# Kernel tuning notes

Hardware: AMD Instinct MI355X
Metric: run time of the kernel (lower is better)

Reference implementation:

```python
import jax, jax.numpy as jnp
import numpy as np

B, S = 32, 256


def _lsa(cost):
    """Rectangular linear sum assignment (Jonker-Volgenant shortest augmenting path),
    equivalent to scipy.optimize.linear_sum_assignment. cost: [R, C] numpy."""
    cost = np.asarray(cost, dtype=np.float64)
    transposed = cost.shape[0] > cost.shape[1]
    if transposed:
        cost = cost.T
    nr, nc = cost.shape  # nr <= nc
    u = np.zeros(nr)
    v = np.zeros(nc)
    path = np.full(nc, -1, dtype=np.int64)
    col4row = np.full(nr, -1, dtype=np.int64)
    row4col = np.full(nc, -1, dtype=np.int64)
    for cur_row in range(nr):
        min_val = 0.0
        i = cur_row
        remaining = np.arange(nc)
        sp = np.full(nc, np.inf)
        SR = np.zeros(nr, dtype=bool)
        SC = np.zeros(nc, dtype=bool)
        sink = -1
        while sink == -1:
            SR[i] = True
            r = min_val + cost[i, remaining] - u[i] - v[remaining]
            better = r < sp[remaining]
            idx_b = remaining[better]
            sp[idx_b] = r[better]
            path[idx_b] = i
            k = int(np.argmin(sp[remaining]))
            j = int(remaining[k])
            min_val = float(sp[j])
            if row4col[j] == -1:
                sink = j
            else:
                i = int(row4col[j])
                SC[j] = True
                remaining = np.delete(remaining, k)
        u[cur_row] += min_val
        others = SR.copy()
        others[cur_row] = False
        rr = np.where(others)[0]
        u[rr] += min_val - sp[col4row[rr]]
        cc = np.where(SC)[0]
        v[cc] += sp[cc] - min_val
        j = sink
        while True:
            i = int(path[j])
            row4col[j] = i
            col4row[i], j = j, int(col4row[i])
            if i == cur_row:
                break
    if transposed:
        rows = col4row
        cols = np.arange(nr)
        order = np.argsort(rows)
        return rows[order], cols[order]
    return np.arange(nr), col4row


def _match(cost_np, valid_np):
    """Per-sample Hungarian matching restricted to valid GT columns.
    Returns padded (pred_idx, gt_idx) [B, maxG] and ngt [B]."""
    Bn = cost_np.shape[0]
    ngt = valid_np.sum(axis=1).astype(np.int64)
    maxG = max(int(ngt.max()), 1)
    pi = np.zeros((Bn, maxG), dtype=np.int64)
    gi = np.zeros((Bn, maxG), dtype=np.int64)
    for b in range(Bn):
        cols = np.where(valid_np[b])[0]
        if len(cols) == 0:
            continue
        r, c = _lsa(cost_np[b][:, cols])
        pi[b, : len(r)] = r
        gi[b, : len(c)] = cols[c]
    return pi, gi, ngt


def _bce_clipped(p, t):
    # matches torch BCELoss: log terms clamped at -100
    return -(t * jnp.clip(jnp.log(p), -100.0) + (1.0 - t) * jnp.clip(jnp.log(1.0 - p), -100.0))


def _loss(pred_strokes, pred_validity, targets, pi, gi, ngt):
    gt_strokes = targets[..., :10]
    gt_val = targets[..., 10:11]
    Bn, maxG = pi.shape
    ngt_f = jnp.asarray(ngt, dtype=pred_strokes.dtype)
    mask = (jnp.arange(maxG)[None, :] < jnp.asarray(ngt)[:, None]).astype(pred_strokes.dtype)  # [B, maxG]
    bidx = np.arange(Bn)[:, None]
    mp = pred_strokes[bidx, pi]  # [B, maxG, 10]
    mg = gt_strokes[bidx, gi]    # [B, maxG, 10]
    # per-sample L1 means over matched pairs (coord: first 8 dims, width: last 2)
    coord = (jnp.abs(mp[..., :8] - mg[..., :8]).sum(-1) * mask).sum(-1) / jnp.maximum(ngt_f * 8.0, 1.0)
    width = (jnp.abs(mp[..., 8:10] - mg[..., 8:10]).sum(-1) * mask).sum(-1) / jnp.maximum(ngt_f * 2.0, 1.0)
    bce = _bce_clipped(pred_validity, gt_val).mean(axis=(1, 2))  # global validity BCE per sample
    # if num_gt == 0 the original only adds the validity BCE
    loss_b = jnp.where(ngt_f > 0, 5.0 * coord + 1.0 * width + 1.0 * bce, bce)
    return loss_b.mean()


def setup_inputs() -> dict:
    key = jax.random.key(0)
    k1, k2, k3, k4 = jax.random.split(key, 4)
    pred_strokes = jax.random.normal(k1, (B, S, 10), dtype=jnp.float32)
    pred_validity = jax.random.uniform(k2, (B, S, 1), dtype=jnp.float32, minval=1e-4, maxval=1.0 - 1e-4)
    gt_strokes = jax.random.normal(k3, (B, S, 10), dtype=jnp.float32)
    gt_valid = (jax.random.uniform(k4, (B, S, 1)) < 0.3).astype(jnp.float32)
    targets = jnp.concatenate([gt_strokes, gt_valid], axis=-1)
    return {"pred_strokes": pred_strokes, "pred_validity": pred_validity, "targets": targets}


def reference(pred_strokes, pred_validity, targets):
    gt_strokes = targets[..., :10]
    gt_val = targets[..., 10:11]
    # vectorized pairwise cost: 5 * L1(coord) + 1 * L1(width), [B, S, S]
    coord_c = jnp.abs(pred_strokes[:, :, None, :8] - gt_strokes[:, None, :, :8]).sum(-1)
    width_c = jnp.abs(pred_strokes[:, :, None, 8:10] - gt_strokes[:, None, :, 8:10]).sum(-1)
    cost = 5.0 * coord_c + width_c
    pi, gi, ngt = _match(np.asarray(cost), np.asarray(gt_val[..., 0]) > 0.5)
    return _loss(pred_strokes, pred_validity, targets, pi, gi, ngt)
```

## Files before the change

### kernel.cpp

```cpp
#include <hip/hip_runtime.h>
#include <math.h>

#define BN 32
#define SN 256
#define CAP 96
#define NT  256

#define KINF 0xFF800000u
#define KMAX 0xFFFFFFFFu
#define CLNONE 0x7FFFFFFF

__device__ __forceinline__ unsigned f2k(float f) {
    unsigned b = __float_as_uint(f);
    return (b & 0x80000000u) ? ~b : (b | 0x80000000u);
}
__device__ __forceinline__ float k2f(unsigned k) {
    unsigned b = (k & 0x80000000u) ? (k ^ 0x80000000u) : ~k;
    return __uint_as_float(b);
}
__device__ __forceinline__ int sel4(int a0, int a1, int a2, int a3, int s) {
    int x01 = (s & 1) ? a1 : a0;
    int x23 = (s & 1) ? a3 : a2;
    return (s & 2) ? x23 : x01;
}
#define DPP_MIN(x, ctrl) do {                                                    \
    unsigned _t = (unsigned)__builtin_amdgcn_update_dpp((int)(x), (int)(x),      \
                                                        (ctrl), 0xF, 0xF, false);\
    if (_t < (x)) (x) = _t;                                                      \
} while (0)
#define DPP_MIN2(m1, m2, ctrl) do {                                              \
    unsigned _o1 = (unsigned)__builtin_amdgcn_update_dpp(-1, (int)(m1),          \
                                                         (ctrl), 0xF, 0xF, false);\
    unsigned _o2 = (unsigned)__builtin_amdgcn_update_dpp(-1, (int)(m2),          \
                                                         (ctrl), 0xF, 0xF, false);\
    unsigned _hi = (m1) > _o1 ? (m1) : _o1;                                      \
    (m1) = (m1) < _o1 ? (m1) : _o1;                                              \
    unsigned _s  = (m2) < _o2 ? (m2) : _o2;                                      \
    (m2) = _s < _hi ? _s : _hi;                                                  \
} while (0)
#define DPP_CHAIN_MIN2(a,b) do { DPP_MIN2(a,b,0x111); DPP_MIN2(a,b,0x112); DPP_MIN2(a,b,0x114); \
                                 DPP_MIN2(a,b,0x118); DPP_MIN2(a,b,0x142); DPP_MIN2(a,b,0x143); } while (0)

__device__ __forceinline__ unsigned waveMinU(unsigned x) {
    DPP_MIN(x, 0x111);
    DPP_MIN(x, 0x112);
    DPP_MIN(x, 0x114);
    DPP_MIN(x, 0x118);
    DPP_MIN(x, 0x142);
    DPP_MIN(x, 0x143);
    return (unsigned)__builtin_amdgcn_readlane((int)x, 63);
}

__device__ __forceinline__ void pickLowest(unsigned long long n0, unsigned long long n1,
                                           unsigned long long n2, unsigned long long n3,
                                           int& lm, int& slot) {
    int l0 = n0 ? __builtin_ctzll(n0) : 64;
    int l1 = n1 ? __builtin_ctzll(n1) : 64;
    int l2 = n2 ? __builtin_ctzll(n2) : 64;
    int l3 = n3 ? __builtin_ctzll(n3) : 64;
    int a  = l0 < l1 ? l0 : l1;
    int c  = l2 < l3 ? l2 : l3;
    lm   = a < c ? a : c;
    slot = (l0 == lm) ? 0 : (l1 == lm) ? 1 : (l2 == lm) ? 2 : 3;
}

__device__ __forceinline__ void waveArgmin(unsigned q0, unsigned q1, unsigned q2,
                                           unsigned q3, unsigned& vk, int& col) {
    unsigned a = q0 < q1 ? q0 : q1;
    unsigned b = q2 < q3 ? q2 : q3;
    unsigned m = a < b ? a : b;
    vk = waveMinU(m);
    unsigned long long n0 = __ballot(q0 == vk);
    unsigned long long n1 = __ballot(q1 == vk);
    unsigned long long n2 = __ballot(q2 == vk);
    unsigned long long n3 = __ballot(q3 == vk);
    int lm, slot;
    pickLowest(n0, n1, n2, n3, lm, slot);
    col = lm * 4 + slot;
}

__device__ __forceinline__ float costf(const float* pb, const float* gc) {
    float c = 0.f;
    #pragma unroll
    for (int d = 0; d < 8; ++d) c += fabsf(pb[d] - gc[d]);
    float w = fabsf(pb[8] - gc[8]) + fabsf(pb[9] - gc[9]);
    return 5.0f * c + w;
}

__global__ __launch_bounds__(NT) void detr_kernel(
    const float* __restrict__ pred_strokes,
    const float* __restrict__ pred_validity,
    const float* __restrict__ targets,
    float* __restrict__ out)
{
    extern __shared__ __align__(16) float sC[];
    __shared__ __align__(16) float sPred[SN * 10];
    __shared__ __align__(16) float sRowC[SN * 10];
    __shared__ float sU[SN];
    __shared__ float sVal[SN];
    __shared__ int   sJ[SN];
    __shared__ int   sClaim[SN];
    __shared__ int   sFree[SN];
    __shared__ int   sCr4[SN];
    __shared__ float sRed[12];
    __shared__ int   sNgt;

    const int b = blockIdx.x, tid = threadIdx.x, lane = tid & 63, wid = tid >> 6;

    {
        const float4* gp = (const float4*)(pred_strokes + (size_t)b * SN * 10);
        float4* sp4 = (float4*)sPred;
        for (int t = tid; t < SN * 10 / 4; t += NT) sp4[t] = gp[t];
        const float4* gt = (const float4*)(targets + (size_t)b * SN * 11);
        float4* st4 = (float4*)sC;
        for (int t = tid; t < SN * 11 / 4; t += NT) st4[t] = gt[t];
        sClaim[tid] = CLNONE;
        sJ[tid]     = 0;
    }
    __syncthreads();

    if (wid == 0) {
        const float* tmpT = sC;
        int ng = 0;
        #pragma unroll
        for (int s = 0; s < 4; ++s) {
            int   pos = s * 64 + lane;
            float tv  = tmpT[pos * 11 + 10];
            sVal[pos] = tv;
            bool  val = tv > 0.5f;
            unsigned long long m = __ballot(val);
            if (val) {
                int r = ng + (int)__popcll(m & ((1ull << lane) - 1ull));
                #pragma unroll
                for (int d = 0; d < 10; ++d) sRowC[r * 10 + d] = tmpT[pos * 11 + d];
            }
            ng += (int)__popcll(m);
        }
        if (lane == 0) sNgt = ng;
    }
    __syncthreads();
    const int ngt = sNgt;

    __align__(16) float prf[40];
    #pragma unroll
    for (int t = 0; t < 10; ++t) ((float4*)prf)[t] = ((const float4*)sPred)[lane * 10 + t];

    float bces;
    {
        float pv  = pred_validity[(size_t)b * SN + tid];
        float tv  = sVal[tid];
        float lp  = logf(pv);       if (lp  < -100.f) lp  = -100.f;
        float l1p = logf(1.f - pv); if (l1p < -100.f) l1p = -100.f;
        bces = -(tv * lp + (1.f - tv) * l1p);
    }

    for (int r = wid; r < ngt; r += 4) {
        const float* gp = &sRowC[r * 10];
        float gc[10];
        #pragma unroll
        for (int d = 0; d < 10; ++d) gc[d] = gp[d];
        float4 cc;
        cc.x = costf(prf +  0, gc);
        cc.y = costf(prf + 10, gc);
        cc.z = costf(prf + 20, gc);
        cc.w = costf(prf + 30, gc);
        if (r < CAP) ((float4*)sC)[r * 64 + lane] = cc;

        unsigned q0 = f2k(cc.x), q1 = f2k(cc.y), q2 = f2k(cc.z), q3 = f2k(cc.w);
        unsigned u1k; int mj;
        waveArgmin(q0, q1, q2, q3, u1k, mj);
        if (lane == 0) {
            sU[r] = k2f(u1k);
            sJ[r] = mj;
            atomicMin(&sClaim[mj], r);
        }
    }
    __syncthreads();

    if (wid == 0) {
        float v0 = 0.f, v1 = 0.f, v2 = 0.f, v3 = 0.f;
        float sc0 = 0.f, sc1 = 0.f, sc2 = 0.f, sc3 = 0.f;
        int   p0 = -1, p1 = -1, p2 = -1, p3 = -1;

        int4 cl = ((const int4*)sClaim)[lane];
        int rv0 = (cl.x != CLNONE) ? cl.x : -1;
        int rv1 = (cl.y != CLNONE) ? cl.y : -1;
        int rv2 = (cl.z != CLNONE) ? cl.z : -1;
        int rv3 = (cl.w != CLNONE) ? cl.w : -1;
        int4 j4 = ((const int4*)sJ)[lane];
        int cr0 = (lane * 4 + 0 < ngt && sClaim[j4.x] == lane * 4 + 0) ? j4.x : -1;
        int cr1 = (lane * 4 + 1 < ngt && sClaim[j4.y] == lane * 4 + 1) ? j4.y : -1;
        int cr2 = (lane * 4 + 2 < ngt && sClaim[j4.z] == lane * 4 + 2) ? j4.z : -1;
        int cr3 = (lane * 4 + 3 < ngt && sClaim[j4.w] == lane * 4 + 3) ? j4.w : -1;

        int nfree = 0;
        #pragma unroll
        for (int s = 0; s < 4; ++s) {
            int  pos = s * 64 + lane;
            bool fr = (pos < ngt) && (sClaim[sJ[pos]] != pos);
            unsigned long long m = __ballot(fr);
            if (fr) sFree[nfree + (int)__popcll(m & ((1ull << lane) - 1ull))] = pos;
            nfree += (int)__popcll(m);
        }

        #define ASSIGN_COL(J, R) { unsigned _m = (lane == ((J) >> 2)) ? (1u << ((J) & 3)) : 0u; \
            rv0 = (_m & 1) ? (R) : rv0; rv1 = (_m & 2) ? (R) : rv1;                             \
            rv2 = (_m & 4) ? (R) : rv2; rv3 = (_m & 8) ? (R) : rv3; }
        #define ASSIGN_ROW(R, J) { unsigned _m = (lane == ((R) >> 2)) ? (1u << ((R) & 3)) : 0u; \
            cr0 = (_m & 1) ? (J) : cr0; cr1 = (_m & 2) ? (J) : cr1;                             \
            cr2 = (_m & 4) ? (J) : cr2; cr3 = (_m & 8) ? (J) : cr3; }
        #define READ_RV(LM, SL) __builtin_amdgcn_readlane(sel4(rv0,rv1,rv2,rv3,(SL)), (LM))
        #define LOADROW(I, CW)                                                   \
            if ((I) < CAP) (CW) = ((const float4*)sC)[(I) * 64 + lane];          \
            else {                                                               \
                float gc[10];                                                    \
                _Pragma("unroll")                                                \
                for (int d = 0; d < 10; ++d) gc[d] = sRowC[(I) * 10 + d];        \
                (CW).x = costf(prf +  0, gc); (CW).y = costf(prf + 10, gc);      \
                (CW).z = costf(prf + 20, gc); (CW).w = costf(prf + 30, gc);      \
            }

        int cnt = nfree;
        for (int pass = 0; pass < 2 && cnt > 0; ++pass) {
            int newc = 0;
            int rN = sFree[0];
            float4 cwN;
            LOADROW(rN, cwN)
            for (int idx = 0; idx < cnt; ++idx) {
                const int r = rN;
                const float4 cw = cwN;
                if (idx + 1 < cnt) {
                    rN = sFree[idx + 1];
                    LOADROW(rN, cwN)
                }
                unsigned q0 = f2k(cw.x - v0), q1 = f2k(cw.y - v1);
                unsigned q2 = f2k(cw.z - v2), q3 = f2k(cw.w - v3);
                unsigned a1 = q0 < q1 ? q0 : q1, a2 = q0 < q1 ? q1 : q0;
                unsigned b1 = q2 < q3 ? q2 : q3, b2 = q2 < q3 ? q3 : q2;
                unsigned m1 = a1 < b1 ? a1 : b1;
                unsigned hi = a1 < b1 ? b1 : a1;
                unsigned l2 = a2 < b2 ? a2 : b2;
                unsigned m2 = l2 < hi ? l2 : hi;
                DPP_CHAIN_MIN2(m1, m2);
                unsigned u1k = (unsigned)__builtin_amdgcn_readlane((int)m1, 63);
                unsigned u2k = (unsigned)__builtin_amdgcn_readlane((int)m2, 63);

                unsigned long long n0 = __ballot(q0 == u1k);
                unsigned long long n1 = __ballot(q1 == u1k);
                unsigned long long n2 = __ballot(q2 == u1k);
                unsigned long long n3 = __ballot(q3 == u1k);
                int lm, slot;
                pickLowest(n0, n1, n2, n3, lm, slot);
                int j1 = lm * 4 + slot;
                int i1 = READ_RV(lm, slot);

                if (u1k != u2k) {
                    float du = k2f(u1k) - k2f(u2k);
                    unsigned _m = (lane == (j1 >> 2)) ? (1u << (j1 & 3)) : 0u;
                    v0 = (_m & 1) ? v0 + du : v0;
                    v1 = (_m & 2) ? v1 + du : v1;
                    v2 = (_m & 4) ? v2 + du : v2;
                    v3 = (_m & 8) ? v3 + du : v3;
                    if (lane == 0) sU[r] = k2f(u2k);
                } else {
                    if (i1 >= 0) {
                        switch (slot) {
                            case 0:  n0 &= ~(1ull << lm); break;
                            case 1:  n1 &= ~(1ull << lm); break;
                            case 2:  n2 &= ~(1ull << lm); break;
                            default: n3 &= ~(1ull << lm); break;
                        }
                        pickLowest(n0, n1, n2, n3, lm, slot);
                        j1 = lm * 4 + slot;
                        i1 = READ_RV(lm, slot);
                    }
                    if (lane == 0) sU[r] = k2f(u1k);
                }

                ASSIGN_COL(j1, r)
                ASSIGN_ROW(r, j1)
                if (i1 >= 0) {
                    if (lane == 0) sFree[newc] = i1;
                    newc++;
                }
            }
            cnt = newc;
        }

        for (int fi = 0; fi < cnt; ++fi) {
            const int cur = sFree[fi];
            unsigned k0 = KINF, k1 = KINF, k2 = KINF, k3 = KINF;
            int   scm  = 0;
            float minv = 0.f;
            int   i    = cur;
            int   sink;

            float4 cw;
            LOADROW(i, cw)
            float ui = sU[i];

            for (;;) {
                #define RELAX(S, CS, KS, PS, VS)                                 \
                {                                                                \
                    float rr = ((minv + CS) - ui) - VS;                          \
                    unsigned kr = f2k(rr);                                       \
                    bool upd = (kr < KS) && !((scm >> S) & 1);                   \
                    if (upd) { KS = kr; PS = i; }                                \
                }
                RELAX(0, cw.x, k0, p0, v0)
                RELAX(1, cw.y, k1, p1, v1)
                RELAX(2, cw.z, k2, p2, v2)
                RELAX(3, cw.w, k3, p3, v3)
                #undef RELAX

                unsigned vk; int bj;
                waveArgmin(k0, k1, k2, k3, vk, bj);
                int lm = bj >> 2, slot = bj & 3;
                int rn = READ_RV(lm, slot);
                minv = k2f(vk);
                if (rn < 0) { sink = bj; break; }
                i = rn;

                float4 cw2;
                LOADROW(i, cw2)
                float ui2 = sU[i];

                unsigned _m = (lane == lm) ? (1u << slot) : 0u;
                scm |= (int)_m;
                k0 = (_m & 1) ? KMAX : k0;  sc0 = (_m & 1) ? minv : sc0;
                k1 = (_m & 2) ? KMAX : k1;  sc1 = (_m & 2) ? minv : sc1;
                k2 = (_m & 4) ? KMAX : k2;  sc2 = (_m & 4) ? minv : sc2;
                k3 = (_m & 8) ? KMAX : k3;  sc3 = (_m & 8) ? minv : sc3;

                cw = cw2; ui = ui2;
            }

            if (lane == 0) sU[cur] += minv;
            if (scm & 1) { sU[rv0] += minv - sc0; v0 += sc0 - minv; }
            if (scm & 2) { sU[rv1] += minv - sc1; v1 += sc1 - minv; }
            if (scm & 4) { sU[rv2] += minv - sc2; v2 += sc2 - minv; }
            if (scm & 8) { sU[rv3] += minv - sc3; v3 += sc3 - minv; }

            int j = sink;
            for (;;) {
                int sj = j & 3, lj = j >> 2;
                int i2 = __builtin_amdgcn_readlane(sel4(p0, p1, p2, p3, sj), lj);
                ASSIGN_COL(j, i2)
                int si = i2 & 3, li = i2 >> 2;
                int tmp = __builtin_amdgcn_readlane(sel4(cr0, cr1, cr2, cr3, si), li);
                ASSIGN_ROW(i2, j)
                j = tmp;
                if (i2 == cur) break;
            }
        }

        ((int4*)sCr4)[lane] = make_int4(cr0, cr1, cr2, cr3);
    }
    __syncthreads();

    float coordv = 0.f, widthv = 0.f;
    if (tid < ngt) {
        int p = sCr4[tid];
        const float* pp = &sPred[p * 10];
        const float* gg = &sRowC[tid * 10];
        float c = 0.f;
        #pragma unroll
        for (int d = 0; d < 8; ++d) c += fabsf(pp[d] - gg[d]);
        coordv = c;
        widthv = fabsf(pp[8] - gg[8]) + fabsf(pp[9] - gg[9]);
    }
    #pragma unroll
    for (int m = 1; m <= 32; m <<= 1) {
        coordv += __shfl_xor(coordv, m, 64);
        widthv += __shfl_xor(widthv, m, 64);
        bces   += __shfl_xor(bces,   m, 64);
    }
    if (lane == 0) {
        sRed[wid * 3 + 0] = coordv;
        sRed[wid * 3 + 1] = widthv;
        sRed[wid * 3 + 2] = bces;
    }
    __syncthreads();
    if (tid == 0) {
        float C = 0.f, W = 0.f, Bc = 0.f;
        #pragma unroll
        for (int w = 0; w < 4; ++w) {
            C += sRed[w * 3 + 0]; W += sRed[w * 3 + 1]; Bc += sRed[w * 3 + 2];
        }
        float bcem = Bc / (float)SN;
        float lb = (ngt > 0)
                 ? (5.f * C / (8.f * (float)ngt) + W / (2.f * (float)ngt) + bcem)
                 : bcem;
        atomicAdd(out, lb * (1.0f / (float)BN));
    }
}

extern "C" void kernel_launch(void* const* d_in, const int* in_sizes, int n_in,
                              void* d_out, int out_size, void* d_ws, size_t ws_size,
                              hipStream_t stream) {
    const float* pred_strokes  = (const float*)d_in[0];
    const float* pred_validity = (const float*)d_in[1];
    const float* targets       = (const float*)d_in[2];
    float* out = (float*)d_out;

    const int dynBytes = CAP * SN * 4;
    (void)hipFuncSetAttribute((const void*)detr_kernel,
                              hipFuncAttributeMaxDynamicSharedMemorySize, dynBytes);
    detr_kernel<<<BN, NT, dynBytes, stream>>>(pred_strokes, pred_validity, targets, out);
}
```

Baseline: 115.4 us.

## Use native float min reductions and restructure JV relax to shorten critical path

Replaces the order-preserving uint key encoding (f2k/k2f) with direct float fminf/fmaxf in the DPP wave reductions and argmin ballots. It also restructures the shortest-augmenting-path inner loop: per-row reduced costs (b0..b3) and their lane minimum are precomputed, so the wave minimum can start from min(mK, minv+mb) before the per-column relax update finishes. This takes the relax step off the serial reduction path. Risks: float compare semantics (NaN, -0) differ from the key ordering, and tie-breaking now relies on exact float equality between recomputed sums.

Measured after the change: 113.6 us. No clear change (-1.6%).

```diff
diff --git a/kernel.cpp b/kernel.cpp
--- a/kernel.cpp
+++ b/kernel.cpp
@@ -6,49 +6,45 @@
 #define CAP 96
 #define NT  256
 
-#define KINF 0xFF800000u
-#define KMAX 0xFFFFFFFFu
+#define INFF __builtin_huge_valf()
 #define CLNONE 0x7FFFFFFF
 
-__device__ __forceinline__ unsigned f2k(float f) {
-    unsigned b = __float_as_uint(f);
-    return (b & 0x80000000u) ? ~b : (b | 0x80000000u);
-}
-__device__ __forceinline__ float k2f(unsigned k) {
-    unsigned b = (k & 0x80000000u) ? (k ^ 0x80000000u) : ~k;
-    return __uint_as_float(b);
-}
 __device__ __forceinline__ int sel4(int a0, int a1, int a2, int a3, int s) {
     int x01 = (s & 1) ? a1 : a0;
     int x23 = (s & 1) ? a3 : a2;
     return (s & 2) ? x23 : x01;
 }
-#define DPP_MIN(x, ctrl) do {                                                    \
-    unsigned _t = (unsigned)__builtin_amdgcn_update_dpp((int)(x), (int)(x),      \
-                                                        (ctrl), 0xF, 0xF, false);\
-    if (_t < (x)) (x) = _t;                                                      \
+__device__ __forceinline__ float readlaneF(float x, int l) {
+    return __uint_as_float((unsigned)__builtin_amdgcn_readlane(__float_as_int(x), l));
+}
+
+#define DPP_FMIN(x, ctrl) do {                                                   \
+    float _t = __uint_as_float((unsigned)__builtin_amdgcn_update_dpp(            \
+        __float_as_int(x), __float_as_int(x), (ctrl), 0xF, 0xF, false));         \
+    (x) = fminf((x), _t);                                                        \
 } while (0)
-#define DPP_MIN2(m1, m2, ctrl) do {                                              \
-    unsigned _o1 = (unsigned)__builtin_amdgcn_update_dpp(-1, (int)(m1),          \
-                                                         (ctrl), 0xF, 0xF, false);\
-    unsigned _o2 = (unsigned)__builtin_amdgcn_update_dpp(-1, (int)(m2),          \
-                                                         (ctrl), 0xF, 0xF, false);\
-    unsigned _hi = (m1) > _o1 ? (m1) : _o1;                                      \
-    (m1) = (m1) < _o1 ? (m1) : _o1;                                              \
-    unsigned _s  = (m2) < _o2 ? (m2) : _o2;                                      \
-    (m2) = _s < _hi ? _s : _hi;                                                  \
+
+#define DPP_FMIN2(m1, m2, ctrl) do {                                             \
+    float _o1 = __uint_as_float((unsigned)__builtin_amdgcn_update_dpp(           \
+        0x7F800000, __float_as_int(m1), (ctrl), 0xF, 0xF, false));               \
+    float _o2 = __uint_as_float((unsigned)__builtin_amdgcn_update_dpp(           \
+        0x7F800000, __float_as_int(m2), (ctrl), 0xF, 0xF, false));               \
+    float _hi = fmaxf((m1), _o1);                                                \
+    (m1) = fminf((m1), _o1);                                                     \
+    (m2) = fminf(fminf((m2), _o2), _hi);                                         \
 } while (0)
-#define DPP_CHAIN_MIN2(a,b) do { DPP_MIN2(a,b,0x111); DPP_MIN2(a,b,0x112); DPP_MIN2(a,b,0x114); \
-                                 DPP_MIN2(a,b,0x118); DPP_MIN2(a,b,0x142); DPP_MIN2(a,b,0x143); } while (0)
-
-__device__ __forceinline__ unsigned waveMinU(unsigned x) {
-    DPP_MIN(x, 0x111);
-    DPP_MIN(x, 0x112);
-    DPP_MIN(x, 0x114);
-    DPP_MIN(x, 0x118);
-    DPP_MIN(x, 0x142);
-    DPP_MIN(x, 0x143);
-    return (unsigned)__builtin_amdgcn_readlane((int)x, 63);
+#define DPP_FCHAIN_MIN2(a,b) do { DPP_FMIN2(a,b,0x111); DPP_FMIN2(a,b,0x112);    \
+                                  DPP_FMIN2(a,b,0x114); DPP_FMIN2(a,b,0x118);    \
+                                  DPP_FMIN2(a,b,0x142); DPP_FMIN2(a,b,0x143); } while (0)
+
+__device__ __forceinline__ float waveMinF(float x) {
+    DPP_FMIN(x, 0x111);
+    DPP_FMIN(x, 0x112);
+    DPP_FMIN(x, 0x114);
+    DPP_FMIN(x, 0x118);
+    DPP_FMIN(x, 0x142);
+    DPP_FMIN(x, 0x143);
+    return readlaneF(x, 63);
 }
 
 __device__ __forceinline__ void pickLowest(unsigned long long n0, unsigned long long n1,
@@ -64,12 +60,10 @@
     slot = (l0 == lm) ? 0 : (l1 == lm) ? 1 : (l2 == lm) ? 2 : 3;
 }
 
-__device__ __forceinline__ void waveArgmin(unsigned q0, unsigned q1, unsigned q2,
-                                           unsigned q3, unsigned& vk, int& col) {
-    unsigned a = q0 < q1 ? q0 : q1;
-    unsigned b = q2 < q3 ? q2 : q3;
-    unsigned m = a < b ? a : b;
-    vk = waveMinU(m);
+__device__ __forceinline__ void waveArgminF(float q0, float q1, float q2, float q3,
+                                            float& vk, int& col) {
+    float m = fminf(fminf(q0, q1), fminf(q2, q3));
+    vk = waveMinF(m);
     unsigned long long n0 = __ballot(q0 == vk);
     unsigned long long n1 = __ballot(q1 == vk);
     unsigned long long n2 = __ballot(q2 == vk);
@@ -166,11 +160,10 @@
         cc.w = costf(prf + 30, gc);
         if (r < CAP) ((float4*)sC)[r * 64 + lane] = cc;
 
-        unsigned q0 = f2k(cc.x), q1 = f2k(cc.y), q2 = f2k(cc.z), q3 = f2k(cc.w);
-        unsigned u1k; int mj;
-        waveArgmin(q0, q1, q2, q3, u1k, mj);
+        float vk; int mj;
+        waveArgminF(cc.x, cc.y, cc.z, cc.w, vk, mj);
         if (lane == 0) {
-            sU[r] = k2f(u1k);
+            sU[r] = vk;
             sJ[r] = mj;
             atomicMin(&sClaim[mj], r);
         }
@@ -233,35 +226,33 @@
                     rN = sFree[idx + 1];
                     LOADROW(rN, cwN)
                 }
-                unsigned q0 = f2k(cw.x - v0), q1 = f2k(cw.y - v1);
-                unsigned q2 = f2k(cw.z - v2), q3 = f2k(cw.w - v3);
-                unsigned a1 = q0 < q1 ? q0 : q1, a2 = q0 < q1 ? q1 : q0;
-                unsigned b1 = q2 < q3 ? q2 : q3, b2 = q2 < q3 ? q3 : q2;
-                unsigned m1 = a1 < b1 ? a1 : b1;
-                unsigned hi = a1 < b1 ? b1 : a1;
-                unsigned l2 = a2 < b2 ? a2 : b2;
-                unsigned m2 = l2 < hi ? l2 : hi;
-                DPP_CHAIN_MIN2(m1, m2);
-                unsigned u1k = (unsigned)__builtin_amdgcn_readlane((int)m1, 63);
-                unsigned u2k = (unsigned)__builtin_amdgcn_readlane((int)m2, 63);
-
-                unsigned long long n0 = __ballot(q0 == u1k);
-                unsigned long long n1 = __ballot(q1 == u1k);
-                unsigned long long n2 = __ballot(q2 == u1k);
-                unsigned long long n3 = __ballot(q3 == u1k);
+                float q0 = cw.x - v0, q1 = cw.y - v1;
+                float q2 = cw.z - v2, q3 = cw.w - v3;
+                float a1 = fminf(q0, q1), a2 = fmaxf(q0, q1);
+                float b1 = fminf(q2, q3), b2 = fmaxf(q2, q3);
+                float m1 = fminf(a1, b1);
+                float m2 = fminf(fminf(a2, b2), fmaxf(a1, b1));
+                DPP_FCHAIN_MIN2(m1, m2);
+                float mn1 = readlaneF(m1, 63);
+                float mn2 = readlaneF(m2, 63);
+
+                unsigned long long n0 = __ballot(q0 == mn1);
+                unsigned long long n1 = __ballot(q1 == mn1);
+                unsigned long long n2 = __ballot(q2 == mn1);
+                unsigned long long n3 = __ballot(q3 == mn1);
                 int lm, slot;
                 pickLowest(n0, n1, n2, n3, lm, slot);
                 int j1 = lm * 4 + slot;
                 int i1 = READ_RV(lm, slot);
 
-                if (u1k != u2k) {
-                    float du = k2f(u1k) - k2f(u2k);
+                if (mn1 != mn2) {
+                    float du = mn1 - mn2;
                     unsigned _m = (lane == (j1 >> 2)) ? (1u << (j1 & 3)) : 0u;
                     v0 = (_m & 1) ? v0 + du : v0;
                     v1 = (_m & 2) ? v1 + du : v1;
                     v2 = (_m & 4) ? v2 + du : v2;
                     v3 = (_m & 8) ? v3 + du : v3;
-                    if (lane == 0) sU[r] = k2f(u2k);
+                    if (lane == 0) sU[r] = mn2;
                 } else {
                     if (i1 >= 0) {
                         switch (slot) {
@@ -274,7 +265,7 @@
                         j1 = lm * 4 + slot;
                         i1 = READ_RV(lm, slot);
                     }
-                    if (lane == 0) sU[r] = k2f(u1k);
+                    if (lane == 0) sU[r] = mn1;
                 }
 
                 ASSIGN_COL(j1, r)
@@ -289,7 +280,8 @@
 
         for (int fi = 0; fi < cnt; ++fi) {
             const int cur = sFree[fi];
-            unsigned k0 = KINF, k1 = KINF, k2 = KINF, k3 = KINF;
+            float K0 = INFF, K1 = INFF, K2 = INFF, K3 = INFF;
+            float mK = INFF;
             int   scm  = 0;
             float minv = 0.f;
             int   i    = cur;
@@ -298,26 +290,34 @@
             float4 cw;
             LOADROW(i, cw)
             float ui = sU[i];
+            float b0 = (cw.x - v0) - ui;
+            float b1 = (cw.y - v1) - ui;
+            float b2 = (cw.z - v2) - ui;
+            float b3 = (cw.w - v3) - ui;
+            float mb = fminf(fminf(b0, b1), fminf(b2, b3));
 
             for (;;) {
-                #define RELAX(S, CS, KS, PS, VS)                                 \
-                {                                                                \
-                    float rr = ((minv + CS) - ui) - VS;                          \
-                    unsigned kr = f2k(rr);                                       \
-                    bool upd = (kr < KS) && !((scm >> S) & 1);                   \
-                    if (upd) { KS = kr; PS = i; }                                \
-                }
-                RELAX(0, cw.x, k0, p0, v0)
-                RELAX(1, cw.y, k1, p1, v1)
-                RELAX(2, cw.z, k2, p2, v2)
-                RELAX(3, cw.w, k3, p3, v3)
-                #undef RELAX
-
-                unsigned vk; int bj;
-                waveArgmin(k0, k1, k2, k3, vk, bj);
-                int lm = bj >> 2, slot = bj & 3;
+                float cand = minv + mb;
+                float m    = fminf(mK, cand);
+                float vk   = waveMinF(m);
+
+                float kr0 = minv + b0, kr1 = minv + b1;
+                float kr2 = minv + b2, kr3 = minv + b3;
+                bool  u0 = kr0 < K0, u1 = kr1 < K1, u2 = kr2 < K2, u3 = kr3 < K3;
+                p0 = u0 ? i : p0; p1 = u1 ? i : p1;
+                p2 = u2 ? i : p2; p3 = u3 ? i : p3;
+                K0 = fminf(K0, kr0); K1 = fminf(K1, kr1);
+                K2 = fminf(K2, kr2); K3 = fminf(K3, kr3);
+
+                unsigned long long n0 = __ballot(K0 == vk);
+                unsigned long long n1 = __ballot(K1 == vk);
+                unsigned long long n2 = __ballot(K2 == vk);
+                unsigned long long n3 = __ballot(K3 == vk);
+                int lm, slot;
+                pickLowest(n0, n1, n2, n3, lm, slot);
+                int bj = lm * 4 + slot;
                 int rn = READ_RV(lm, slot);
-                minv = k2f(vk);
+                minv = vk;
                 if (rn < 0) { sink = bj; break; }
                 i = rn;
 
@@ -327,12 +327,17 @@
 
                 unsigned _m = (lane == lm) ? (1u << slot) : 0u;
                 scm |= (int)_m;
-                k0 = (_m & 1) ? KMAX : k0;  sc0 = (_m & 1) ? minv : sc0;
-                k1 = (_m & 2) ? KMAX : k1;  sc1 = (_m & 2) ? minv : sc1;
-                k2 = (_m & 4) ? KMAX : k2;  sc2 = (_m & 4) ? minv : sc2;
-                k3 = (_m & 8) ? KMAX : k3;  sc3 = (_m & 8) ? minv : sc3;
-
-                cw = cw2; ui = ui2;
+                K0 = (_m & 1) ? INFF : K0;  sc0 = (_m & 1) ? minv : sc0;
+                K1 = (_m & 2) ? INFF : K1;  sc1 = (_m & 2) ? minv : sc1;
+                K2 = (_m & 4) ? INFF : K2;  sc2 = (_m & 4) ? minv : sc2;
+                K3 = (_m & 8) ? INFF : K3;  sc3 = (_m & 8) ? minv : sc3;
+                mK = fminf(fminf(K0, K1), fminf(K2, K3));
+
+                b0 = (scm & 1) ? INFF : (cw2.x - v0) - ui2;
+                b1 = (scm & 2) ? INFF : (cw2.y - v1) - ui2;
+                b2 = (scm & 4) ? INFF : (cw2.z - v2) - ui2;
+                b3 = (scm & 8) ? INFF : (cw2.w - v3) - ui2;
+                mb = fminf(fminf(b0, b1), fminf(b2, b3));
             }
 
             if (lane == 0) sU[cur] += minv;
```

## Speculatively prefetch second-best row in augmenting path; drop auction prefetch

Applied to the files above, without the earlier changes.

In the shortest-augmenting-path loop, the argmin now computes both the smallest and second-smallest keys with a DPP reduction. The row owning the second-smallest column is prefetched from the shared cost cache, on the bet that it becomes the next row visited after the current column is scanned. In the auction/greedy pass, the software prefetch of the next free row is removed and each row is loaded in place. This trades extra ballots and LDS loads per iteration for hiding LDS latency on the serial critical path, and it may waste work when the speculation misses.

Result: slower. 120.9 us (+4.8%).

```diff
diff --git a/kernel.cpp b/kernel.cpp
--- a/kernel.cpp
+++ b/kernel.cpp
@@ -223,16 +223,10 @@
         int cnt = nfree;
         for (int pass = 0; pass < 2 && cnt > 0; ++pass) {
             int newc = 0;
-            int rN = sFree[0];
-            float4 cwN;
-            LOADROW(rN, cwN)
             for (int idx = 0; idx < cnt; ++idx) {
-                const int r = rN;
-                const float4 cw = cwN;
-                if (idx + 1 < cnt) {
-                    rN = sFree[idx + 1];
-                    LOADROW(rN, cwN)
-                }
+                const int r = sFree[idx];
+                float4 cw;
+                LOADROW(r, cw)
                 unsigned q0 = f2k(cw.x - v0), q1 = f2k(cw.y - v1);
                 unsigned q2 = f2k(cw.z - v2), q3 = f2k(cw.w - v3);
                 unsigned a1 = q0 < q1 ? q0 : q1, a2 = q0 < q1 ? q1 : q0;
@@ -294,6 +288,9 @@
             float minv = 0.f;
             int   i    = cur;
             int   sink;
+            int   specRow = -1;
+            float4 cwS;
+            float  uiS = 0.f;
 
             float4 cw;
             LOADROW(i, cw)
@@ -313,17 +310,34 @@
                 RELAX(3, cw.w, k3, p3, v3)
                 #undef RELAX
 
-                unsigned vk; int bj;
-                waveArgmin(k0, k1, k2, k3, vk, bj);
-                int lm = bj >> 2, slot = bj & 3;
+                unsigned a1 = k0 < k1 ? k0 : k1, a2 = k0 < k1 ? k1 : k0;
+                unsigned b1 = k2 < k3 ? k2 : k3, b2 = k2 < k3 ? k3 : k2;
+                unsigned m1 = a1 < b1 ? a1 : b1;
+                unsigned hi = a1 < b1 ? b1 : a1;
+                unsigned l2 = a2 < b2 ? a2 : b2;
+                unsigned m2 = l2 < hi ? l2 : hi;
+                DPP_CHAIN_MIN2(m1, m2);
+                unsigned u1k = (unsigned)__builtin_amdgcn_readlane((int)m1, 63);
+                unsigned u2k = (unsigned)__builtin_amdgcn_readlane((int)m2, 63);
+
+                unsigned long long n0 = __ballot(k0 == u1k);
+                unsigned long long n1 = __ballot(k1 == u1k);
+                unsigned long long n2 = __ballot(k2 == u1k);
+                unsigned long long n3 = __ballot(k3 == u1k);
+                int lm, slot;
+                pickLowest(n0, n1, n2, n3, lm, slot);
+                int bj = lm * 4 + slot;
                 int rn = READ_RV(lm, slot);
-                minv = k2f(vk);
+                minv = k2f(u1k);
                 if (rn < 0) { sink = bj; break; }
                 i = rn;
 
-                float4 cw2;
-                LOADROW(i, cw2)
-                float ui2 = sU[i];
+                if (i == specRow) {
+                    cw = cwS; ui = uiS;
+                } else {
+                    LOADROW(i, cw)
+                    ui = sU[i];
+                }
 
                 unsigned _m = (lane == lm) ? (1u << slot) : 0u;
                 scm |= (int)_m;
@@ -332,7 +346,23 @@
                 k2 = (_m & 4) ? KMAX : k2;  sc2 = (_m & 4) ? minv : sc2;
                 k3 = (_m & 8) ? KMAX : k3;  sc3 = (_m & 8) ? minv : sc3;
 
-                cw = cw2; ui = ui2;
+                specRow = -1;
+                if (u2k < KINF) {
+                    unsigned long long s0 = __ballot(k0 == u2k);
+                    unsigned long long s1 = __ballot(k1 == u2k);
+                    unsigned long long s2 = __ballot(k2 == u2k);
+                    unsigned long long s3 = __ballot(k3 == u2k);
+                    if ((s0 | s1 | s2 | s3) != 0ull) {
+                        int lm2, sl2;
+                        pickLowest(s0, s1, s2, s3, lm2, sl2);
+                        int rn2 = READ_RV(lm2, sl2);
+                        if (rn2 >= 0 && rn2 < CAP) {
+                            cwS = ((const float4*)sC)[rn2 * 64 + lane];
+                            uiS = sU[rn2];
+                            specRow = rn2;
+                        }
+                    }
+                }
             }
 
             if (lane == 0) sU[cur] += minv;
```
